# Optimization experiments

Hardware: AMD Instinct MI355X
Metric: run time of the kernel (lower is better)

Reference implementation:

```python
import jax, jax.numpy as jnp
import numpy as np

DT_MIN, DT_MAX = 1e-3, 1e-1
LN_EPS = 1e-5


def layernorm(x, w, b):
    mu = jnp.mean(x, axis=-1, keepdims=True)
    var = jnp.mean(jnp.square(x - mu), axis=-1, keepdims=True)
    return (x - mu) * jax.lax.rsqrt(var + LN_EPS) * w + b


def _scan(Lam_bar, Bu, reverse=False):
    # Lam_bar: (P,) complex64; Bu: (B, L, P) complex64
    A = jnp.broadcast_to(Lam_bar, Bu.shape)

    def binop(e_i, e_j):
        a_i, b_i = e_i
        a_j, b_j = e_j
        return a_j * a_i, a_j * b_i + b_j

    _, xs = jax.lax.associative_scan(binop, (A, Bu), axis=1, reverse=reverse)
    return xs  # (B, L, P)


def s5_ssm(u, Lambda_re, Lambda_im, log_step, B_re, B_im, C_re, C_im, D):
    # u: (B, L, H) real. Diagonal S5 with ZOH discretization, bidirectional.
    step = jnp.exp(log_step)                          # (P,)
    Lam = (Lambda_re + 1j * Lambda_im).astype(jnp.complex64)
    Lam_bar = jnp.exp(Lam * step)                     # (P,)
    Bmat = (B_re + 1j * B_im).astype(jnp.complex64)   # (P, H)
    B_bar = ((Lam_bar - 1.0) / Lam)[:, None] * Bmat   # (P, H)
    Bu = jnp.einsum('blh,ph->blp', u.astype(jnp.complex64), B_bar)  # (B,L,P)
    xs_f = _scan(Lam_bar, Bu, reverse=False)
    xs_b = _scan(Lam_bar, Bu, reverse=True)
    xs = jnp.concatenate([xs_f, xs_b], axis=-1)       # (B, L, 2P)
    C = (C_re + 1j * C_im).astype(jnp.complex64)      # (H, 2P)
    ys = 2.0 * jnp.einsum('hp,blp->blh', C, xs).real  # conj-symmetric output
    return ys + D * u


def gelu(x):
    return jax.nn.gelu(x, approximate=False)  # torch default (erf) gelu


def s5_block(x, ln1_w, ln1_b, ln2_w, ln2_b, Lambda_re, Lambda_im, log_step,
             B_re, B_im, C_re, C_im, D, ff_enc_w, ff_dec_w):
    # attention-style half: pre-LN + S5 + gelu + residual (residual = normed input)
    fx = layernorm(x, ln1_w, ln1_b)
    res = fx
    x = gelu(s5_ssm(fx, Lambda_re, Lambda_im, log_step, B_re, B_im, C_re, C_im, D)) + res
    # FFN half: pre-LN + GEGLU + residual (residual = normed input)
    fx = layernorm(x, ln2_w, ln2_b)
    res = fx
    h = fx @ ff_enc_w.T                               # (B, L, 2*dim)
    a, g = jnp.split(h, 2, axis=-1)
    x = (a * gelu(g)) @ ff_dec_w.T + res
    return x


def setup_inputs() -> dict:
    B, L, D_IN, DIM, P = 4, 4096, 512, 1024, 512
    key = jax.random.key(0)
    ks = jax.random.split(key, 16)
    inp = {}
    inp['x'] = jax.random.normal(ks[0], (B, L, D_IN), dtype=jnp.float32)
    inp['W_in'] = jax.random.normal(ks[1], (DIM, D_IN), jnp.float32) / np.sqrt(D_IN)
    inp['W_out'] = jax.random.normal(ks[2], (D_IN, DIM), jnp.float32) / np.sqrt(DIM)
    inp['ln1_w'] = jnp.ones((DIM,), jnp.float32)
    inp['ln1_b'] = jnp.zeros((DIM,), jnp.float32)
    inp['ln2_w'] = jnp.ones((DIM,), jnp.float32)
    inp['ln2_b'] = jnp.zeros((DIM,), jnp.float32)
    inp['Lambda_re'] = -0.5 * jnp.exp(jax.random.normal(ks[3], (P,), jnp.float32))
    inp['Lambda_im'] = jnp.pi * jax.random.normal(ks[4], (P,), jnp.float32)
    inp['log_step'] = jax.random.uniform(ks[5], (P,), jnp.float32,
                                         minval=np.log(DT_MIN), maxval=np.log(DT_MAX))
    inp['B_re'] = jax.random.normal(ks[6], (P, DIM), jnp.float32) / np.sqrt(DIM)
    inp['B_im'] = jax.random.normal(ks[7], (P, DIM), jnp.float32) / np.sqrt(DIM)
    inp['C_re'] = jax.random.normal(ks[8], (DIM, 2 * P), jnp.float32) / np.sqrt(2 * P)
    inp['C_im'] = jax.random.normal(ks[9], (DIM, 2 * P), jnp.float32) / np.sqrt(2 * P)
    inp['D'] = jax.random.normal(ks[10], (DIM,), jnp.float32)
    inp['ff_enc_w'] = jax.random.normal(ks[11], (2 * DIM, DIM), jnp.float32) / np.sqrt(DIM)
    inp['ff_dec_w'] = jax.random.normal(ks[12], (DIM, DIM), jnp.float32) / np.sqrt(DIM)
    return inp


def reference(x, W_in, W_out, ln1_w, ln1_b, ln2_w, ln2_b, Lambda_re, Lambda_im,
              log_step, B_re, B_im, C_re, C_im, D, ff_enc_w, ff_dec_w):
    h = x @ W_in.T                                    # (B, L, dim)
    h = s5_block(h, ln1_w, ln1_b, ln2_w, ln2_b, Lambda_re, Lambda_im, log_step,
                 B_re, B_im, C_re, C_im, D, ff_enc_w, ff_dec_w)
    return h @ W_out.T                                # (B, L, d_input)
```

## Files before the change

### kernel.cpp

```cpp
#include <hip/hip_runtime.h>
#include <cstdint>

typedef __bf16 bf16;
typedef __bf16 bf16x2 __attribute__((ext_vector_type(2)));
typedef __bf16 bf16x4 __attribute__((ext_vector_type(4)));
typedef __bf16 bf16x8 __attribute__((ext_vector_type(8)));
typedef float f32x4 __attribute__((ext_vector_type(4)));

#define MROWS 16384
#define DIMH 1024
#define PDIM 512
#define LSEQ 4096
#define CL 16
#define NC (LSEQ / CL)

typedef const __attribute__((address_space(1))) unsigned int* gas_t;
typedef __attribute__((address_space(3))) unsigned int* las_t;

__device__ __forceinline__ float gelu_f(float x) {
  return 0.5f * x * (1.0f + erff(x * 0.70710678118654752f));
}

__global__ void k_prep(const float* __restrict__ Lre, const float* __restrict__ Lim,
                       const float* __restrict__ lstep,
                       float2* __restrict__ lamb, float2* __restrict__ coef) {
  const int p = blockIdx.x * blockDim.x + threadIdx.x;
  if (p >= PDIM) return;
  const float lre = Lre[p], lim = Lim[p];
  const float st = expf(lstep[p]);
  const float er = expf(lre * st);
  const float lbr = er * cosf(lim * st);
  const float lbi = er * sinf(lim * st);
  lamb[p] = make_float2(lbr, lbi);
  const float ar = lbr - 1.0f, ai = lbi;
  const float d = lre * lre + lim * lim;
  coef[p] = make_float2((ar * lre + ai * lim) / d, (ai * lre - ar * lim) / d);
}

__global__ void k_f32_to_bf16(const float* __restrict__ in, bf16* __restrict__ outp, int n) {
  const int i = (blockIdx.x * 256 + threadIdx.x) * 4;
  if (i >= n) return;
  const float4 v = *(const float4*)(in + i);
  bf16x4 o = { (bf16)v.x, (bf16)v.y, (bf16)v.z, (bf16)v.w };
  *(bf16x4*)(outp + i) = o;
}

__global__ void k_bcat(const float* __restrict__ Bre, const float* __restrict__ Bim,
                       const float2* __restrict__ coef, bf16* __restrict__ bcat) {
  const int idx = blockIdx.x * 256 + threadIdx.x;
  const int p = idx >> 10;
  const float2 c = coef[p];
  const float br = Bre[idx], bi = Bim[idx];
  bcat[idx] = (bf16)(c.x * br - c.y * bi);
  bcat[idx + PDIM * DIMH] = (bf16)(c.x * bi + c.y * br);
}

__global__ void k_ccomb(const float* __restrict__ Cre, const float* __restrict__ Cim,
                        bf16* __restrict__ cc) {
  const int idx = blockIdx.x * 256 + threadIdx.x;
  const int n = idx >> 11, k = idx & 2047;
  float v;
  if (k < 512)       v =  2.0f * Cre[n * 1024 + k];
  else if (k < 1024) v = -2.0f * Cim[n * 1024 + (k - 512)];
  else if (k < 1536) v =  2.0f * Cre[n * 1024 + 512 + (k - 1024)];
  else               v = -2.0f * Cim[n * 1024 + 512 + (k - 1536)];
  cc[idx] = (bf16)v;
}


#define VMCNT4 asm volatile("s_waitcnt vmcnt(4)" ::: "memory")
#define VMCNT0 asm volatile("s_waitcnt vmcnt(0)" ::: "memory")
#define LGKM0  asm volatile("s_waitcnt lgkmcnt(0)" ::: "memory")
#define SCHED0 __builtin_amdgcn_sched_barrier(0)
#define BAR    __builtin_amdgcn_s_barrier()

#define PHASE(slot, kh, mh, LOADB, STAGE_STMT, WAIT_STMT)                      \
  {                                                                            \
    if (LOADB) ldB(slot, kh, bfr);                                             \
    ldA(slot, kh, mh, afr);                                                    \
    STAGE_STMT;                                                                \
    SCHED0;                                                                    \
    BAR;                                                                       \
    LGKM0;                                                                     \
    SCHED0;                                                                    \
    __builtin_amdgcn_s_setprio(1);                                             \
    _Pragma("unroll")                                                          \
    for (int m = 0; m < 4; ++m)                                                \
      _Pragma("unroll")                                                        \
      for (int n = 0; n < 4; ++n)                                              \
        acc[(mh) * 4 + m][n] = __builtin_amdgcn_mfma_f32_16x16x32_bf16(        \
            afr[m], bfr[n], acc[(mh) * 4 + m][n], 0, 0, 0);                    \
    __builtin_amdgcn_s_setprio(0);                                             \
    SCHED0;                                                                    \
    WAIT_STMT;                                                                 \
    BAR;                                                                       \
  }

template <int EPI>
__global__ __launch_bounds__(512, 2) void k_gemm(const bf16* __restrict__ A,
                                                 const bf16* __restrict__ W,
                                                 float* __restrict__ Cf,
                                                 bf16* __restrict__ Cb,
                                                 const float* __restrict__ auxf,
                                                 const bf16* __restrict__ auxb,
                                                 int K, int N, int nbnl) {
  extern __shared__ char lds[];
  const int q = (int)gridDim.x >> 3;
  const int s = ((int)blockIdx.x & 7) * q + ((int)blockIdx.x >> 3);
  const int bm = s >> nbnl;
  const int bn = s & ((1 << nbnl) - 1);
  const int tid = threadIdx.x;
  const int lane = tid & 63;
  const int wave = tid >> 6;
  const int wr = wave >> 2;
  const int wc = wave & 3;

  const size_t arow0 = (size_t)bm * 256;
  const size_t wrow0 = (size_t)bn * 256;
  const int srow = tid >> 2;
  const int schunk = (tid & 3) ^ ((tid >> 3) & 3);
  const int wbase = wave << 10;

  f32x4 acc[8][4];
#pragma unroll
  for (int i = 0; i < 8; ++i)
#pragma unroll
    for (int j = 0; j < 4; ++j) acc[i][j] = (f32x4){0.f, 0.f, 0.f, 0.f};

  auto stage = [&](int slot, int kh, int kt) {
    const int kcol = kt * 64 + kh * 32 + schunk * 8;
    {
      char* base = lds + slot * 32768 + kh * 16384;
      __builtin_amdgcn_global_load_lds(
          (gas_t)(A + (arow0 + srow) * (size_t)K + kcol), (las_t)(base + wbase), 16, 0, 0);
      __builtin_amdgcn_global_load_lds(
          (gas_t)(A + (arow0 + 128 + srow) * (size_t)K + kcol), (las_t)(base + 8192 + wbase), 16, 0, 0);
    }
    {
      char* base = lds + 65536 + slot * 32768 + kh * 16384;
      __builtin_amdgcn_global_load_lds(
          (gas_t)(W + (wrow0 + srow) * (size_t)K + kcol), (las_t)(base + wbase), 16, 0, 0);
      __builtin_amdgcn_global_load_lds(
          (gas_t)(W + (wrow0 + 128 + srow) * (size_t)K + kcol), (las_t)(base + 8192 + wbase), 16, 0, 0);
    }
  };

  auto ldA = [&](int slot, int kh, int mh, bf16x8* af) {
#pragma unroll
    for (int m = 0; m < 4; ++m) {
      const int row = wr * 128 + mh * 64 + m * 16 + (lane & 15);
      const int pc = (lane >> 4) ^ ((row >> 1) & 3);
      af[m] = *(const bf16x8*)(lds + slot * 32768 + kh * 16384 + row * 64 + pc * 16);
    }
  };
  auto ldB = [&](int slot, int kh, bf16x8* bf) {
#pragma unroll
    for (int n = 0; n < 4; ++n) {
      const int row = wc * 64 + n * 16 + (lane & 15);
      const int pc = (lane >> 4) ^ ((row >> 1) & 3);
      bf[n] = *(const bf16x8*)(lds + 65536 + slot * 32768 + kh * 16384 + row * 64 + pc * 16);
    }
  };

  bf16x8 afr[4], bfr[4];

  stage(0, 0, 0);
  stage(0, 1, 0);
  stage(1, 0, 1);
  VMCNT4;
  BAR;

  const int NT = K >> 7;
  for (int t = 0; t < NT; ++t) {
    const int nl = (t + 1 < NT);
    PHASE(0, 0, 0, 1, stage(1, 1, 2 * t + 1), (void)0);
    PHASE(0, 0, 1, 0, (void)0, (void)0);
    PHASE(0, 1, 0, 1, if (nl) stage(0, 0, 2 * t + 2), (void)0);
    if (nl) { PHASE(0, 1, 1, 0, (void)0, VMCNT4); }
    else    { PHASE(0, 1, 1, 0, (void)0, VMCNT0); }
    PHASE(1, 0, 0, 1, if (nl) stage(0, 1, 2 * t + 2), (void)0);
    PHASE(1, 0, 1, 0, (void)0, (void)0);
    PHASE(1, 1, 0, 1, if (nl) stage(1, 0, 2 * t + 3), (void)0);
    if (nl) { PHASE(1, 1, 1, 0, (void)0, VMCNT4); }
    else    { PHASE(1, 1, 1, 0, (void)0, (void)0); }
  }

  const int n0 = (int)wrow0 + wc * 64 + (lane & 15);
  const size_t m0 = arow0 + wr * 128 + ((lane >> 4) << 2);
#pragma unroll
  for (int mi = 0; mi < 8; ++mi)
#pragma unroll
    for (int n = 0; n < 4; ++n) {
      const size_t mb = m0 + mi * 16;
      const int nn = n0 + n * 16;
#pragma unroll
      for (int r = 0; r < 4; ++r) {
        const size_t idx = (mb + r) * (size_t)N + nn;
        const float v = acc[mi][n][r];
        if constexpr (EPI == 0) {
          Cf[idx] = v;
        } else if constexpr (EPI == 1) {
          Cb[idx] = (bf16)((float)auxb[idx] * gelu_f(v));
        } else if constexpr (EPI == 2) {
          Cb[idx] = (bf16)(v + auxf[idx]);
        } else {
          Cb[idx] = (bf16)v;
        }
      }
    }
}

__global__ __launch_bounds__(256) void k_ln(const float* __restrict__ X,
                                            const float* __restrict__ w,
                                            const float* __restrict__ bb,
                                            float* __restrict__ Yf, bf16* __restrict__ Yb) {
  const int m = blockIdx.x;
  const int tid = threadIdx.x;
  const float4 v = ((const float4*)(X + (size_t)m * DIMH))[tid];
  float s = v.x + v.y + v.z + v.w;
  float s2 = v.x * v.x + v.y * v.y + v.z * v.z + v.w * v.w;
#pragma unroll
  for (int off = 32; off > 0; off >>= 1) { s += __shfl_down(s, off); s2 += __shfl_down(s2, off); }
  __shared__ float rs[4], rq[4];
  if ((tid & 63) == 0) { rs[tid >> 6] = s; rq[tid >> 6] = s2; }
  __syncthreads();
  s = rs[0] + rs[1] + rs[2] + rs[3];
  s2 = rq[0] + rq[1] + rq[2] + rq[3];
  const float mu = s * (1.0f / DIMH);
  const float inv = rsqrtf(s2 * (1.0f / DIMH) - mu * mu + 1e-5f);
  const float4 wv = ((const float4*)w)[tid];
  const float4 bv = ((const float4*)bb)[tid];
  const float o0 = (v.x - mu) * inv * wv.x + bv.x;
  const float o1 = (v.y - mu) * inv * wv.y + bv.y;
  const float o2 = (v.z - mu) * inv * wv.z + bv.z;
  const float o3 = (v.w - mu) * inv * wv.w + bv.w;
  ((float4*)(Yf + (size_t)m * DIMH))[tid] = make_float4(o0, o1, o2, o3);
  bf16x4 ob = { (bf16)o0, (bf16)o1, (bf16)o2, (bf16)o3 };
  *(bf16x4*)(Yb + (size_t)m * DIMH + tid * 4) = ob;
}

__global__ __launch_bounds__(256) void k_ln2e(const float* __restrict__ YS,
                                              const float* __restrict__ FX,
                                              const float* __restrict__ Dv,
                                              const float* __restrict__ w,
                                              const float* __restrict__ bb,
                                              float* __restrict__ Yf, bf16* __restrict__ Yb) {
  const int m = blockIdx.x;
  const int tid = threadIdx.x;
  const float4 ys = ((const float4*)(YS + (size_t)m * DIMH))[tid];
  const float4 fx = ((const float4*)(FX + (size_t)m * DIMH))[tid];
  const float4 dv = ((const float4*)Dv)[tid];
  const float t0 = gelu_f(ys.x + dv.x * fx.x) + fx.x;
  const float t1 = gelu_f(ys.y + dv.y * fx.y) + fx.y;
  const float t2 = gelu_f(ys.z + dv.z * fx.z) + fx.z;
  const float t3 = gelu_f(ys.w + dv.w * fx.w) + fx.w;
  float s = t0 + t1 + t2 + t3;
  float s2 = t0 * t0 + t1 * t1 + t2 * t2 + t3 * t3;
#pragma unroll
  for (int off = 32; off > 0; off >>= 1) { s += __shfl_down(s, off); s2 += __shfl_down(s2, off); }
  __shared__ float rs[4], rq[4];
  if ((tid & 63) == 0) { rs[tid >> 6] = s; rq[tid >> 6] = s2; }
  __syncthreads();
  s = rs[0] + rs[1] + rs[2] + rs[3];
  s2 = rq[0] + rq[1] + rq[2] + rq[3];
  const float mu = s * (1.0f / DIMH);
  const float inv = rsqrtf(s2 * (1.0f / DIMH) - mu * mu + 1e-5f);
  const float4 wv = ((const float4*)w)[tid];
  const float4 bv = ((const float4*)bb)[tid];
  const float o0 = (t0 - mu) * inv * wv.x + bv.x;
  const float o1 = (t1 - mu) * inv * wv.y + bv.y;
  const float o2 = (t2 - mu) * inv * wv.z + bv.z;
  const float o3 = (t3 - mu) * inv * wv.w + bv.w;
  ((float4*)(Yf + (size_t)m * DIMH))[tid] = make_float4(o0, o1, o2, o3);
  bf16x4 ob = { (bf16)o0, (bf16)o1, (bf16)o2, (bf16)o3 };
  *(bf16x4*)(Yb + (size_t)m * DIMH + tid * 4) = ob;
}

__global__ __launch_bounds__(256) void k_scanA(const float* __restrict__ Bu,
                                               const float2* __restrict__ lamb,
                                               float2* __restrict__ carry) {
  const int bc = blockIdx.x;
  const int b = bc >> 8, c = bc & (NC - 1);
  const int t = threadIdx.x;
  const size_t rbase = ((size_t)b * LSEQ + (size_t)c * CL) * DIMH;
  float2 re[CL], im[CL];
#pragma unroll
  for (int i = 0; i < CL; ++i) {
    re[i] = *(const float2*)(Bu + rbase + (size_t)i * DIMH + 2 * t);
    im[i] = *(const float2*)(Bu + rbase + (size_t)i * DIMH + PDIM + 2 * t);
  }
  const float2 l0 = lamb[2 * t];
  const float2 l1 = lamb[2 * t + 1];
  const size_t cb = ((size_t)bc * 2) * PDIM;
  {
    float s0r = 0.f, s0i = 0.f, s1r = 0.f, s1i = 0.f;
#pragma unroll
    for (int i = 0; i < CL; ++i) {
      float nr = l0.x * s0r - l0.y * s0i + re[i].x;
      float ni = l0.x * s0i + l0.y * s0r + im[i].x;
      s0r = nr; s0i = ni;
      nr = l1.x * s1r - l1.y * s1i + re[i].y;
      ni = l1.x * s1i + l1.y * s1r + im[i].y;
      s1r = nr; s1i = ni;
    }
    carry[cb + 2 * t]     = make_float2(s0r, s0i);
    carry[cb + 2 * t + 1] = make_float2(s1r, s1i);
  }
  {
    float s0r = 0.f, s0i = 0.f, s1r = 0.f, s1i = 0.f;
#pragma unroll
    for (int i = CL - 1; i >= 0; --i) {
      float nr = l0.x * s0r - l0.y * s0i + re[i].x;
      float ni = l0.x * s0i + l0.y * s0r + im[i].x;
      s0r = nr; s0i = ni;
      nr = l1.x * s1r - l1.y * s1i + re[i].y;
      ni = l1.x * s1i + l1.y * s1r + im[i].y;
      s1r = nr; s1i = ni;
    }
    carry[cb + PDIM + 2 * t]     = make_float2(s0r, s0i);
    carry[cb + PDIM + 2 * t + 1] = make_float2(s1r, s1i);
  }
}

__global__ __launch_bounds__(256) void k_scanB(const float2* __restrict__ carry,
                                               const float2* __restrict__ lamb,
                                               float2* __restrict__ seed) {
  const int b = blockIdx.x;
  const int t = threadIdx.x;
  const float2 l0 = lamb[2 * t], l1 = lamb[2 * t + 1];
  float L0r = l0.x, L0i = l0.y, L1r = l1.x, L1i = l1.y;
#pragma unroll
  for (int q = 0; q < 4; ++q) {
    float tr = L0r * L0r - L0i * L0i; L0i = 2.f * L0r * L0i; L0r = tr;
    tr = L1r * L1r - L1i * L1i; L1i = 2.f * L1r * L1i; L1r = tr;
  }
  float S0r = 0.f, S0i = 0.f, S1r = 0.f, S1i = 0.f;
  for (int c = 0; c < NC; ++c) {
    const size_t base = (((size_t)b * NC + c) * 2) * PDIM;
    const float2 c0 = carry[base + 2 * t];
    const float2 c1 = carry[base + 2 * t + 1];
    seed[base + 2 * t]     = make_float2(S0r, S0i);
    seed[base + 2 * t + 1] = make_float2(S1r, S1i);
    float nr = L0r * S0r - L0i * S0i + c0.x;
    float ni = L0r * S0i + L0i * S0r + c0.y;
    S0r = nr; S0i = ni;
    nr = L1r * S1r - L1i * S1i + c1.x;
    ni = L1r * S1i + L1i * S1r + c1.y;
    S1r = nr; S1i = ni;
  }
  S0r = 0.f; S0i = 0.f; S1r = 0.f; S1i = 0.f;
  for (int c = NC - 1; c >= 0; --c) {
    const size_t base = (((size_t)b * NC + c) * 2) * PDIM + PDIM;
    const float2 c0 = carry[base + 2 * t];
    const float2 c1 = carry[base + 2 * t + 1];
    seed[base + 2 * t]     = make_float2(S0r, S0i);
    seed[base + 2 * t + 1] = make_float2(S1r, S1i);
    float nr = L0r * S0r - L0i * S0i + c0.x;
    float ni = L0r * S0i + L0i * S0r + c0.y;
    S0r = nr; S0i = ni;
    nr = L1r * S1r - L1i * S1i + c1.x;
    ni = L1r * S1i + L1i * S1r + c1.y;
    S1r = nr; S1i = ni;
  }
}

__global__ __launch_bounds__(256) void k_scanC(const float* __restrict__ Bu,
                                               const float2* __restrict__ lamb,
                                               const float2* __restrict__ seed,
                                               bf16* __restrict__ xs) {
  const int bc = blockIdx.x;
  const int b = bc >> 8, c = bc & (NC - 1);
  const int t = threadIdx.x;
  const size_t rbase = ((size_t)b * LSEQ + (size_t)c * CL) * DIMH;
  float2 re[CL], im[CL];
#pragma unroll
  for (int i = 0; i < CL; ++i) {
    re[i] = *(const float2*)(Bu + rbase + (size_t)i * DIMH + 2 * t);
    im[i] = *(const float2*)(Bu + rbase + (size_t)i * DIMH + PDIM + 2 * t);
  }
  const float2 l0 = lamb[2 * t];
  const float2 l1 = lamb[2 * t + 1];
  const size_t sb = ((size_t)bc * 2) * PDIM;
  const size_t obase = ((size_t)b * LSEQ + (size_t)c * CL) * 2048;
  {
    const float2 s0 = seed[sb + 2 * t];
    const float2 s1 = seed[sb + 2 * t + 1];
    float s0r = s0.x, s0i = s0.y, s1r = s1.x, s1i = s1.y;
#pragma unroll
    for (int i = 0; i < CL; ++i) {
      float nr = l0.x * s0r - l0.y * s0i + re[i].x;
      float ni = l0.x * s0i + l0.y * s0r + im[i].x;
      s0r = nr; s0i = ni;
      nr = l1.x * s1r - l1.y * s1i + re[i].y;
      ni = l1.x * s1i + l1.y * s1r + im[i].y;
      s1r = nr; s1i = ni;
      bf16x2 wr2 = { (bf16)s0r, (bf16)s1r };
      bf16x2 wi2 = { (bf16)s0i, (bf16)s1i };
      *(bf16x2*)(xs + obase + (size_t)i * 2048 + 2 * t) = wr2;
      *(bf16x2*)(xs + obase + (size_t)i * 2048 + PDIM + 2 * t) = wi2;
    }
  }
  {
    const float2 s0 = seed[sb + PDIM + 2 * t];
    const float2 s1 = seed[sb + PDIM + 2 * t + 1];
    float s0r = s0.x, s0i = s0.y, s1r = s1.x, s1i = s1.y;
#pragma unroll
    for (int i = CL - 1; i >= 0; --i) {
      float nr = l0.x * s0r - l0.y * s0i + re[i].x;
      float ni = l0.x * s0i + l0.y * s0r + im[i].x;
      s0r = nr; s0i = ni;
      nr = l1.x * s1r - l1.y * s1i + re[i].y;
      ni = l1.x * s1i + l1.y * s1r + im[i].y;
      s1r = nr; s1i = ni;
      bf16x2 wr2 = { (bf16)s0r, (bf16)s1r };
      bf16x2 wi2 = { (bf16)s0i, (bf16)s1i };
      *(bf16x2*)(xs + obase + (size_t)i * 2048 + 1024 + 2 * t) = wr2;
      *(bf16x2*)(xs + obase + (size_t)i * 2048 + 1536 + 2 * t) = wi2;
    }
  }
}

extern "C" void kernel_launch(void* const* d_in, const int* in_sizes, int n_in,
                              void* d_out, int out_size, void* d_ws, size_t ws_size,
                              hipStream_t stream) {
  const float* x    = (const float*)d_in[0];
  const float* W_in = (const float*)d_in[1];
  const float* W_out= (const float*)d_in[2];
  const float* ln1w = (const float*)d_in[3];
  const float* ln1b = (const float*)d_in[4];
  const float* ln2w = (const float*)d_in[5];
  const float* ln2b = (const float*)d_in[6];
  const float* Lre  = (const float*)d_in[7];
  const float* Lim  = (const float*)d_in[8];
  const float* lstep= (const float*)d_in[9];
  const float* Bre  = (const float*)d_in[10];
  const float* Bim  = (const float*)d_in[11];
  const float* Cre  = (const float*)d_in[12];
  const float* Cim  = (const float*)d_in[13];
  const float* Dv   = (const float*)d_in[14];
  const float* ffe  = (const float*)d_in[15];
  const float* ffd  = (const float*)d_in[16];
  float* out = (float*)d_out;
  char* ws = (char*)d_ws;

  bf16* winb   = (bf16*)(ws);
  bf16* woutb  = (bf16*)(ws + (1u << 20));
  bf16* bcat   = (bf16*)(ws + (2u << 20));
  bf16* ccomb  = (bf16*)(ws + (4u << 20));
  bf16* ffeb   = (bf16*)(ws + (8u << 20));
  bf16* ffdb   = (bf16*)(ws + (12u << 20));
  float2* lamb = (float2*)(ws + (14u << 20));
  float2* coef = (float2*)(ws + (14u << 20) + 8192);
  bf16* E      = (bf16*)(ws + (16u << 20));
  float2* carry = (float2*)(ws + (16u << 20));
  float2* seed  = (float2*)(ws + (24u << 20));
  float* Abuf  = (float*)(ws + (48u << 20));
  float* Bbuf  = (float*)(ws + (112u << 20));
  float* Cbuf  = (float*)(ws + (176u << 20));
  bf16* xsb    = (bf16*)Cbuf;
  bf16* a_b    = (bf16*)Cbuf;
  bf16* G      = ((bf16*)Cbuf) + 16777216;

  static bool attr_done = false;
  if (!attr_done) {
    hipFuncSetAttribute((const void*)&k_gemm<0>, hipFuncAttributeMaxDynamicSharedMemorySize, 131072);
    hipFuncSetAttribute((const void*)&k_gemm<1>, hipFuncAttributeMaxDynamicSharedMemorySize, 131072);
    hipFuncSetAttribute((const void*)&k_gemm<2>, hipFuncAttributeMaxDynamicSharedMemorySize, 131072);
    hipFuncSetAttribute((const void*)&k_gemm<3>, hipFuncAttributeMaxDynamicSharedMemorySize, 131072);
    attr_done = true;
  }

  k_prep<<<2, 256, 0, stream>>>(Lre, Lim, lstep, lamb, coef);
  k_f32_to_bf16<<<512, 256, 0, stream>>>(W_in, winb, 524288);
  k_f32_to_bf16<<<512, 256, 0, stream>>>(W_out, woutb, 524288);
  k_f32_to_bf16<<<2048, 256, 0, stream>>>(ffe, ffeb, 2097152);
  k_f32_to_bf16<<<1024, 256, 0, stream>>>(ffd, ffdb, 1048576);
  k_f32_to_bf16<<<8192, 256, 0, stream>>>(x, E, 8388608);
  k_bcat<<<2048, 256, 0, stream>>>(Bre, Bim, coef, bcat);
  k_ccomb<<<8192, 256, 0, stream>>>(Cre, Cim, ccomb);

  k_gemm<0><<<256, 512, 131072, stream>>>(E, winb, Abuf, nullptr, nullptr, nullptr, 512, 1024, 2);
  k_ln<<<16384, 256, 0, stream>>>(Abuf, ln1w, ln1b, Bbuf, E);
  k_gemm<0><<<256, 512, 131072, stream>>>(E, bcat, Abuf, nullptr, nullptr, nullptr, 1024, 1024, 2);
  k_scanA<<<4 * NC, 256, 0, stream>>>(Abuf, lamb, carry);
  k_scanB<<<4, 256, 0, stream>>>(carry, lamb, seed);
  k_scanC<<<4 * NC, 256, 0, stream>>>(Abuf, lamb, seed, xsb);
  k_gemm<0><<<256, 512, 131072, stream>>>(xsb, ccomb, Abuf, nullptr, nullptr, nullptr, 2048, 1024, 2);
  k_ln2e<<<16384, 256, 0, stream>>>(Abuf, Bbuf, Dv, ln2w, ln2b, Bbuf, E);
  k_gemm<3><<<256, 512, 131072, stream>>>(E, ffeb, nullptr, a_b, nullptr, nullptr, 1024, 1024, 2);
  k_gemm<1><<<256, 512, 131072, stream>>>(E, ffeb + (size_t)1024 * 1024, nullptr, G, nullptr, a_b, 1024, 1024, 2);
  k_gemm<2><<<256, 512, 131072, stream>>>(G, ffdb, nullptr, E, Bbuf, nullptr, 1024, 1024, 2);
  k_gemm<0><<<128, 512, 131072, stream>>>(E, woutb, out, nullptr, nullptr, nullptr, 1024, 512, 1);
}
```

Measured before the change: 519.1 us.

## Store all intermediate activations in bf16 instead of fp32

GEMM outputs that feed later stages (the W_in projection, Bu, ys, and the FFN residual) are now written as bf16 rather than fp32. The layernorm and scan kernels read bf16 inputs, and the residual is carried as the bf16 normalized tensor instead of a separate fp32 copy. The workspace layout is reorganized to match. This roughly halves activation memory traffic between kernels and drops the extra fp32 stores, at the cost of lower precision in the scan inputs and the residual path.

```diff
diff --git a/kernel.cpp b/kernel.cpp
--- a/kernel.cpp
+++ b/kernel.cpp
@@ -101,7 +101,6 @@
                                                  const bf16* __restrict__ W,
                                                  float* __restrict__ Cf,
                                                  bf16* __restrict__ Cb,
-                                                 const float* __restrict__ auxf,
                                                  const bf16* __restrict__ auxb,
                                                  int K, int N, int nbnl) {
   extern __shared__ char lds[];
@@ -202,7 +201,7 @@
         } else if constexpr (EPI == 1) {
           Cb[idx] = (bf16)((float)auxb[idx] * gelu_f(v));
         } else if constexpr (EPI == 2) {
-          Cb[idx] = (bf16)(v + auxf[idx]);
+          Cb[idx] = (bf16)(v + (float)auxb[idx]);
         } else {
           Cb[idx] = (bf16)v;
         }
@@ -210,15 +209,16 @@
     }
 }
 
-__global__ __launch_bounds__(256) void k_ln(const float* __restrict__ X,
+__global__ __launch_bounds__(256) void k_ln(const bf16* __restrict__ X,
                                             const float* __restrict__ w,
                                             const float* __restrict__ bb,
-                                            float* __restrict__ Yf, bf16* __restrict__ Yb) {
+                                            bf16* __restrict__ Yb) {
   const int m = blockIdx.x;
   const int tid = threadIdx.x;
-  const float4 v = ((const float4*)(X + (size_t)m * DIMH))[tid];
-  float s = v.x + v.y + v.z + v.w;
-  float s2 = v.x * v.x + v.y * v.y + v.z * v.z + v.w * v.w;
+  const bf16x4 v4 = *(const bf16x4*)(X + (size_t)m * DIMH + tid * 4);
+  const float v0 = (float)v4[0], v1 = (float)v4[1], v2 = (float)v4[2], v3 = (float)v4[3];
+  float s = v0 + v1 + v2 + v3;
+  float s2 = v0 * v0 + v1 * v1 + v2 * v2 + v3 * v3;
 #pragma unroll
   for (int off = 32; off > 0; off >>= 1) { s += __shfl_down(s, off); s2 += __shfl_down(s2, off); }
   __shared__ float rs[4], rq[4];
@@ -230,30 +230,26 @@
   const float inv = rsqrtf(s2 * (1.0f / DIMH) - mu * mu + 1e-5f);
   const float4 wv = ((const float4*)w)[tid];
   const float4 bv = ((const float4*)bb)[tid];
-  const float o0 = (v.x - mu) * inv * wv.x + bv.x;
-  const float o1 = (v.y - mu) * inv * wv.y + bv.y;
-  const float o2 = (v.z - mu) * inv * wv.z + bv.z;
-  const float o3 = (v.w - mu) * inv * wv.w + bv.w;
-  ((float4*)(Yf + (size_t)m * DIMH))[tid] = make_float4(o0, o1, o2, o3);
-  bf16x4 ob = { (bf16)o0, (bf16)o1, (bf16)o2, (bf16)o3 };
+  bf16x4 ob = { (bf16)((v0 - mu) * inv * wv.x + bv.x), (bf16)((v1 - mu) * inv * wv.y + bv.y),
+                (bf16)((v2 - mu) * inv * wv.z + bv.z), (bf16)((v3 - mu) * inv * wv.w + bv.w) };
   *(bf16x4*)(Yb + (size_t)m * DIMH + tid * 4) = ob;
 }
 
-__global__ __launch_bounds__(256) void k_ln2e(const float* __restrict__ YS,
-                                              const float* __restrict__ FX,
+__global__ __launch_bounds__(256) void k_ln2e(const bf16* __restrict__ YS,
+                                              bf16* FXE,
                                               const float* __restrict__ Dv,
                                               const float* __restrict__ w,
-                                              const float* __restrict__ bb,
-                                              float* __restrict__ Yf, bf16* __restrict__ Yb) {
+                                              const float* __restrict__ bb) {
   const int m = blockIdx.x;
   const int tid = threadIdx.x;
-  const float4 ys = ((const float4*)(YS + (size_t)m * DIMH))[tid];
-  const float4 fx = ((const float4*)(FX + (size_t)m * DIMH))[tid];
+  const bf16x4 ys4 = *(const bf16x4*)(YS + (size_t)m * DIMH + tid * 4);
+  const bf16x4 fx4 = *(const bf16x4*)(FXE + (size_t)m * DIMH + tid * 4);
   const float4 dv = ((const float4*)Dv)[tid];
-  const float t0 = gelu_f(ys.x + dv.x * fx.x) + fx.x;
-  const float t1 = gelu_f(ys.y + dv.y * fx.y) + fx.y;
-  const float t2 = gelu_f(ys.z + dv.z * fx.z) + fx.z;
-  const float t3 = gelu_f(ys.w + dv.w * fx.w) + fx.w;
+  const float f0 = (float)fx4[0], f1 = (float)fx4[1], f2 = (float)fx4[2], f3 = (float)fx4[3];
+  const float t0 = gelu_f((float)ys4[0] + dv.x * f0) + f0;
+  const float t1 = gelu_f((float)ys4[1] + dv.y * f1) + f1;
+  const float t2 = gelu_f((float)ys4[2] + dv.z * f2) + f2;
+  const float t3 = gelu_f((float)ys4[3] + dv.w * f3) + f3;
   float s = t0 + t1 + t2 + t3;
   float s2 = t0 * t0 + t1 * t1 + t2 * t2 + t3 * t3;
 #pragma unroll
@@ -267,16 +263,12 @@
   const float inv = rsqrtf(s2 * (1.0f / DIMH) - mu * mu + 1e-5f);
   const float4 wv = ((const float4*)w)[tid];
   const float4 bv = ((const float4*)bb)[tid];
-  const float o0 = (t0 - mu) * inv * wv.x + bv.x;
-  const float o1 = (t1 - mu) * inv * wv.y + bv.y;
-  const float o2 = (t2 - mu) * inv * wv.z + bv.z;
-  const float o3 = (t3 - mu) * inv * wv.w + bv.w;
-  ((float4*)(Yf + (size_t)m * DIMH))[tid] = make_float4(o0, o1, o2, o3);
-  bf16x4 ob = { (bf16)o0, (bf16)o1, (bf16)o2, (bf16)o3 };
-  *(bf16x4*)(Yb + (size_t)m * DIMH + tid * 4) = ob;
-}
-
-__global__ __launch_bounds__(256) void k_scanA(const float* __restrict__ Bu,
+  bf16x4 ob = { (bf16)((t0 - mu) * inv * wv.x + bv.x), (bf16)((t1 - mu) * inv * wv.y + bv.y),
+                (bf16)((t2 - mu) * inv * wv.z + bv.z), (bf16)((t3 - mu) * inv * wv.w + bv.w) };
+  *(bf16x4*)(FXE + (size_t)m * DIMH + tid * 4) = ob;
+}
+
+__global__ __launch_bounds__(256) void k_scanA(const bf16* __restrict__ Bu,
                                                const float2* __restrict__ lamb,
                                                float2* __restrict__ carry) {
   const int bc = blockIdx.x;
@@ -286,8 +278,10 @@
   float2 re[CL], im[CL];
 #pragma unroll
   for (int i = 0; i < CL; ++i) {
-    re[i] = *(const float2*)(Bu + rbase + (size_t)i * DIMH + 2 * t);
-    im[i] = *(const float2*)(Bu + rbase + (size_t)i * DIMH + PDIM + 2 * t);
+    const bf16x2 r2 = *(const bf16x2*)(Bu + rbase + (size_t)i * DIMH + 2 * t);
+    const bf16x2 i2 = *(const bf16x2*)(Bu + rbase + (size_t)i * DIMH + PDIM + 2 * t);
+    re[i] = make_float2((float)r2[0], (float)r2[1]);
+    im[i] = make_float2((float)i2[0], (float)i2[1]);
   }
   const float2 l0 = lamb[2 * t];
   const float2 l1 = lamb[2 * t + 1];
@@ -364,7 +358,7 @@
   }
 }
 
-__global__ __launch_bounds__(256) void k_scanC(const float* __restrict__ Bu,
+__global__ __launch_bounds__(256) void k_scanC(const bf16* __restrict__ Bu,
                                                const float2* __restrict__ lamb,
                                                const float2* __restrict__ seed,
                                                bf16* __restrict__ xs) {
@@ -375,8 +369,10 @@
   float2 re[CL], im[CL];
 #pragma unroll
   for (int i = 0; i < CL; ++i) {
-    re[i] = *(const float2*)(Bu + rbase + (size_t)i * DIMH + 2 * t);
-    im[i] = *(const float2*)(Bu + rbase + (size_t)i * DIMH + PDIM + 2 * t);
+    const bf16x2 r2 = *(const bf16x2*)(Bu + rbase + (size_t)i * DIMH + 2 * t);
+    const bf16x2 i2 = *(const bf16x2*)(Bu + rbase + (size_t)i * DIMH + PDIM + 2 * t);
+    re[i] = make_float2((float)r2[0], (float)r2[1]);
+    im[i] = make_float2((float)i2[0], (float)i2[1]);
   }
   const float2 l0 = lamb[2 * t];
   const float2 l1 = lamb[2 * t + 1];
@@ -452,14 +448,15 @@
   float2* lamb = (float2*)(ws + (14u << 20));
   float2* coef = (float2*)(ws + (14u << 20) + 8192);
   bf16* E      = (bf16*)(ws + (16u << 20));
-  float2* carry = (float2*)(ws + (16u << 20));
-  float2* seed  = (float2*)(ws + (24u << 20));
-  float* Abuf  = (float*)(ws + (48u << 20));
-  float* Bbuf  = (float*)(ws + (112u << 20));
-  float* Cbuf  = (float*)(ws + (176u << 20));
-  bf16* xsb    = (bf16*)Cbuf;
-  bf16* a_b    = (bf16*)Cbuf;
-  bf16* G      = ((bf16*)Cbuf) + 16777216;
+  bf16* hb     = (bf16*)(ws + (48u << 20));
+  bf16* Bub    = (bf16*)(ws + (48u << 20));
+  bf16* ysb    = (bf16*)(ws + (48u << 20));
+  bf16* x3b    = (bf16*)(ws + (48u << 20));
+  bf16* xsb    = (bf16*)(ws + (80u << 20));
+  bf16* a_b    = (bf16*)(ws + (80u << 20));
+  bf16* G      = (bf16*)(ws + (112u << 20));
+  float2* carry = (float2*)(ws + (144u << 20));
+  float2* seed  = (float2*)(ws + (152u << 20));
 
   static bool attr_done = false;
   if (!attr_done) {
@@ -479,16 +476,16 @@
   k_bcat<<<2048, 256, 0, stream>>>(Bre, Bim, coef, bcat);
   k_ccomb<<<8192, 256, 0, stream>>>(Cre, Cim, ccomb);
 
-  k_gemm<0><<<256, 512, 131072, stream>>>(E, winb, Abuf, nullptr, nullptr, nullptr, 512, 1024, 2);
-  k_ln<<<16384, 256, 0, stream>>>(Abuf, ln1w, ln1b, Bbuf, E);
-  k_gemm<0><<<256, 512, 131072, stream>>>(E, bcat, Abuf, nullptr, nullptr, nullptr, 1024, 1024, 2);
-  k_scanA<<<4 * NC, 256, 0, stream>>>(Abuf, lamb, carry);
+  k_gemm<3><<<256, 512, 131072, stream>>>(E, winb, nullptr, hb, nullptr, 512, 1024, 2);
+  k_ln<<<16384, 256, 0, stream>>>(hb, ln1w, ln1b, E);
+  k_gemm<3><<<256, 512, 131072, stream>>>(E, bcat, nullptr, Bub, nullptr, 1024, 1024, 2);
+  k_scanA<<<4 * NC, 256, 0, stream>>>(Bub, lamb, carry);
   k_scanB<<<4, 256, 0, stream>>>(carry, lamb, seed);
-  k_scanC<<<4 * NC, 256, 0, stream>>>(Abuf, lamb, seed, xsb);
-  k_gemm<0><<<256, 512, 131072, stream>>>(xsb, ccomb, Abuf, nullptr, nullptr, nullptr, 2048, 1024, 2);
-  k_ln2e<<<16384, 256, 0, stream>>>(Abuf, Bbuf, Dv, ln2w, ln2b, Bbuf, E);
-  k_gemm<3><<<256, 512, 131072, stream>>>(E, ffeb, nullptr, a_b, nullptr, nullptr, 1024, 1024, 2);
-  k_gemm<1><<<256, 512, 131072, stream>>>(E, ffeb + (size_t)1024 * 1024, nullptr, G, nullptr, a_b, 1024, 1024, 2);
-  k_gemm<2><<<256, 512, 131072, stream>>>(G, ffdb, nullptr, E, Bbuf, nullptr, 1024, 1024, 2);
-  k_gemm<0><<<128, 512, 131072, stream>>>(E, woutb, out, nullptr, nullptr, nullptr, 1024, 512, 1);
-}
+  k_scanC<<<4 * NC, 256, 0, stream>>>(Bub, lamb, seed, xsb);
+  k_gemm<3><<<256, 512, 131072, stream>>>(xsb, ccomb, nullptr, ysb, nullptr, 2048, 1024, 2);
+  k_ln2e<<<16384, 256, 0, stream>>>(ysb, E, Dv, ln2w, ln2b);
+  k_gemm<3><<<256, 512, 131072, stream>>>(E, ffeb, nullptr, a_b, nullptr, 1024, 1024, 2);
+  k_gemm<1><<<256, 512, 131072, stream>>>(E, ffeb + (size_t)1024 * 1024, nullptr, G, a_b, 1024, 1024, 2);
+  k_gemm<2><<<256, 512, 131072, stream>>>(G, ffdb, nullptr, x3b, E, 1024, 1024, 2);
+  k_gemm<0><<<128, 512, 131072, stream>>>(x3b, woutb, out, nullptr, nullptr, 1024, 512, 1);
+}
```

After: 477.0 us. 8.1% less time.
